# Optimization experiments

Measured on AMD Instinct MI355X. Metric: run time of the kernel, lower is better.

Reference implementation:

```python
import jax, jax.numpy as jnp
import numpy as np
from jax import lax


def _dw_conv(x, w, dilation):
    # depthwise dilated conv along width; x: [B,H,W,C], w: [1,K,1,C] (HWIO, groups=C)
    return lax.conv_general_dilated(
        x, w,
        window_strides=(1, 1),
        padding='SAME',
        rhs_dilation=(1, dilation),
        dimension_numbers=('NHWC', 'HWIO', 'NHWC'),
        feature_group_count=x.shape[-1])


def setup_inputs() -> dict:
    key = jax.random.key(0)
    kx, k1, k2, k3 = jax.random.split(key, 4)
    B, H, W, C = 16, 21, 4096, 64
    K = 8
    scale = 1.0 / np.sqrt(K)  # keep activations O(1) across stages
    x = jax.random.normal(kx, (B, H, W, C), dtype=jnp.float32)
    w1 = jax.random.normal(k1, (1, K, 1, C), dtype=jnp.float32) * scale
    w2 = jax.random.normal(k2, (1, K, 1, C), dtype=jnp.float32) * scale
    w3 = jax.random.normal(k3, (1, K, 1, C), dtype=jnp.float32) * scale
    return {'x': x, 'w1': w1, 'w2': w2, 'w3': w3}


def reference(x, w1, w2, w3):
    # per-channel Conv2D stack == depthwise conv stack; dilations 1, 2, 4; relu after each
    y = jax.nn.relu(_dw_conv(x, w1, 1))
    y = jax.nn.relu(_dw_conv(y, w2, 2))
    y = jax.nn.relu(_dw_conv(y, w3, 4))
    return y
```

## Files before the change

kernel.cpp:

```cpp
#include <hip/hip_runtime.h>


#define W_DIM   4096
#define C_DIM   64
#define L_CHUNK 256
#define NCHUNK  16
#define NROWS   336
#define WAVES_PER_BLOCK 4

#define S1_BODY(j) do {                                                     \
    float a_ = 0.f;                                                         \
    _Pragma("unroll")                                                       \
    for (int k = 0; k < 8; ++k)                                             \
        a_ = fmaf(xf[((j) - 7 + k + 32) & 15], w1r[k], a_);                 \
    s1f[((j) - 4 + 32) & 15] = fmaxf(a_, 0.f);                              \
} while (0)

#define S2_BODY(j) do {                                                     \
    float a_ = 0.f;                                                         \
    _Pragma("unroll")                                                       \
    for (int k = 0; k < 8; ++k)                                             \
        a_ = fmaf(s1f[((j) - 18 + 2 * k + 32) & 15], w2r[k], a_);           \
    s2f[((j) - 11 + 32) & 31] = fmaxf(a_, 0.f);                             \
} while (0)

#define S3_STORE(j, dst) do {                                               \
    float a_ = 0.f;                                                         \
    _Pragma("unroll")                                                       \
    for (int k = 0; k < 8; ++k)                                             \
        a_ = fmaf(s2f[((j) - 39 + 4 * k + 64) & 31], w3r[k], a_);           \
    (dst) = fmaxf(a_, 0.f);                                                 \
} while (0)

__global__ __launch_bounds__(256, 4)
void splitconv_fused_kernel(const float* __restrict__ x,
                            const float* __restrict__ w1,
                            const float* __restrict__ w2,
                            const float* __restrict__ w3,
                            float* __restrict__ out) {
    const int lane  = threadIdx.x & 63;
    const int wid   = threadIdx.x >> 6;
    const int chunk = blockIdx.x & (NCHUNK - 1);
    const int row   = (blockIdx.x >> 4) * WAVES_PER_BLOCK + wid;
    const int w0    = chunk * L_CHUNK;
    const int c     = lane;

    const float* __restrict__ xrow = x   + (size_t)row * (W_DIM * C_DIM) + c;
    float* __restrict__       orow = out + (size_t)row * (W_DIM * C_DIM) + c;

    float w1r[8], w2r[8], w3r[8];
#pragma unroll
    for (int k = 0; k < 8; ++k) {
        w1r[k] = w1[k * C_DIM + c];
        w2r[k] = w2[k * C_DIM + c];
        w3r[k] = w3[k * C_DIM + c];
    }

    float xf[16], s1f[16], s2f[32];
#pragma unroll
    for (int i = 0; i < 16; ++i) { xf[i] = 0.f; s1f[i] = 0.f; }
#pragma unroll
    for (int i = 0; i < 32; ++i) s2f[i] = 0.f;

    if (chunk >= 1 && chunk <= 14) {
        const float* __restrict__ xp = xrow + (size_t)(w0 - 24) * C_DIM;
        float* __restrict__       op = orow + (size_t)w0 * C_DIM;

#pragma unroll
        for (int j = 0; j < 32; ++j) {
            xf[(j + 8) & 15] = xp[j * C_DIM];
            if (j >= 15) S1_BODY(j);
            if (j >= 29) S2_BODY(j);
        }
        xp += 32 * C_DIM;

#pragma unroll
        for (int j = 0; j < 32; ++j) {
            xf[(j + 8) & 15] = xp[j * C_DIM];
            S1_BODY(j);
            S2_BODY(j);
            if (j >= 25) S3_STORE(j, op[(j - 25) * C_DIM]);
        }
        xp += 32 * C_DIM;
        op += 7 * C_DIM;

#pragma unroll 1
        for (int g = 2; g <= 8; ++g) {
#pragma unroll
            for (int j = 0; j < 32; ++j) {
                xf[(j + 8) & 15] = xp[j * C_DIM];
                S1_BODY(j);
                S2_BODY(j);
                S3_STORE(j, op[j * C_DIM]);
            }
            xp += 32 * C_DIM;
            op += 32 * C_DIM;
        }

#pragma unroll
        for (int j = 0; j < 32; ++j) {
            if (j <= 16) xf[(j + 8) & 15] = xp[j * C_DIM];
            if (j <= 24) { S1_BODY(j); S2_BODY(j); }
            if (j <  25) S3_STORE(j, op[j * C_DIM]);
        }
    } else {
        for (int g = 0; g < 10; ++g) {
            const int tbase = w0 - 32 + g * 32;
#pragma unroll
            for (int j = 0; j < 32; ++j) {
                const int t = tbase + j;

                {
                    const int z = t + 8;
                    float xv = 0.f;
                    if (z >= 0 && z < W_DIM && (z - w0) <= L_CHUNK + 24)
                        xv = xrow[(size_t)z * C_DIM];
                    xf[(j + 8) & 15] = xv;
                }

                {
                    const int v = t - 4;
                    float a = 0.f;
#pragma unroll
                    for (int k = 0; k < 8; ++k)
                        a = fmaf(xf[(j - 7 + k + 32) & 15], w1r[k], a);
                    float s = fmaxf(a, 0.f);
                    s1f[(j - 4 + 32) & 15] = (v >= 0 && v < W_DIM) ? s : 0.f;
                }

                {
                    const int u = t - 11;
                    float a = 0.f;
#pragma unroll
                    for (int k = 0; k < 8; ++k)
                        a = fmaf(s1f[(j - 18 + 2 * k + 32) & 15], w2r[k], a);
                    float s = fmaxf(a, 0.f);
                    s2f[(j - 11 + 32) & 31] = (u >= 0 && u < W_DIM) ? s : 0.f;
                }

                {
                    const int wq = t - 25;
                    if (wq >= w0 && wq < w0 + L_CHUNK) {
                        float a = 0.f;
#pragma unroll
                        for (int k = 0; k < 8; ++k)
                            a = fmaf(s2f[(j - 39 + 4 * k + 64) & 31], w3r[k], a);
                        orow[(size_t)wq * C_DIM] = fmaxf(a, 0.f);
                    }
                }
            }
        }
    }
}

extern "C" void kernel_launch(void* const* d_in, const int* in_sizes, int n_in,
                              void* d_out, int out_size, void* d_ws, size_t ws_size,
                              hipStream_t stream) {
    const float* x  = (const float*)d_in[0];
    const float* w1 = (const float*)d_in[1];
    const float* w2 = (const float*)d_in[2];
    const float* w3 = (const float*)d_in[3];
    float* out = (float*)d_out;

    const int totalWaves = NROWS * NCHUNK;
    const int blocks = totalWaves / WAVES_PER_BLOCK;
    splitconv_fused_kernel<<<blocks, 256, 0, stream>>>(x, w1, w2, w3, out);
}
```

Measured before the change: 640.8 us.

## Double-buffer input rows in registers, use nontemporal stores, relax occupancy bound

The interior-chunk path now loads x in full 32-element register tiles (xa/xb ping-pong) one group ahead, replacing the 16-entry ring that fetched each element just before use. This puts more loads in flight to hide global memory latency. Output stores become nontemporal to avoid polluting cache with write-once data. Launch bounds drop from 4 to 3 blocks per CU to give the larger register footprint room, which lowers occupancy.

```diff
diff --git a/kernel.cpp b/kernel.cpp
--- a/kernel.cpp
+++ b/kernel.cpp
@@ -8,11 +8,14 @@
 #define NROWS   336
 #define WAVES_PER_BLOCK 4
 
-#define S1_BODY(j) do {                                                     \
+#define S1X(j, CUR, PRV) do {                                               \
     float a_ = 0.f;                                                         \
     _Pragma("unroll")                                                       \
-    for (int k = 0; k < 8; ++k)                                             \
-        a_ = fmaf(xf[((j) - 7 + k + 32) & 15], w1r[k], a_);                 \
+    for (int k = 0; k < 8; ++k) {                                           \
+        const int i_ = (j) - 7 + k;                                         \
+        const float xv_ = (i_ >= 0) ? CUR[i_ & 31] : PRV[(i_ + 32) & 31];   \
+        a_ = fmaf(xv_, w1r[k], a_);                                         \
+    }                                                                       \
     s1f[((j) - 4 + 32) & 15] = fmaxf(a_, 0.f);                              \
 } while (0)
 
@@ -24,15 +27,15 @@
     s2f[((j) - 11 + 32) & 31] = fmaxf(a_, 0.f);                             \
 } while (0)
 
-#define S3_STORE(j, dst) do {                                               \
+#define S3_NT(j, pdst) do {                                                 \
     float a_ = 0.f;                                                         \
     _Pragma("unroll")                                                       \
     for (int k = 0; k < 8; ++k)                                             \
         a_ = fmaf(s2f[((j) - 39 + 4 * k + 64) & 31], w3r[k], a_);           \
-    (dst) = fmaxf(a_, 0.f);                                                 \
+    __builtin_nontemporal_store(fmaxf(a_, 0.f), (pdst));                    \
 } while (0)
 
-__global__ __launch_bounds__(256, 4)
+__global__ __launch_bounds__(256, 3)
 void splitconv_fused_kernel(const float* __restrict__ x,
                             const float* __restrict__ w1,
                             const float* __restrict__ w2,
@@ -56,54 +59,78 @@
         w3r[k] = w3[k * C_DIM + c];
     }
 
-    float xf[16], s1f[16], s2f[32];
+    float s1f[16], s2f[32];
 #pragma unroll
-    for (int i = 0; i < 16; ++i) { xf[i] = 0.f; s1f[i] = 0.f; }
+    for (int i = 0; i < 16; ++i) s1f[i] = 0.f;
 #pragma unroll
     for (int i = 0; i < 32; ++i) s2f[i] = 0.f;
 
     if (chunk >= 1 && chunk <= 14) {
-        const float* __restrict__ xp = xrow + (size_t)(w0 - 24) * C_DIM;
+        float xa[32], xb[32];
+        const float* __restrict__ xp = xrow + (size_t)(w0 - 32) * C_DIM;
         float* __restrict__       op = orow + (size_t)w0 * C_DIM;
 
 #pragma unroll
+        for (int j = 0; j < 32; ++j) xa[j] = xp[j * C_DIM];
+        xp += 32 * C_DIM;
+
+#pragma unroll
         for (int j = 0; j < 32; ++j) {
-            xf[(j + 8) & 15] = xp[j * C_DIM];
-            if (j >= 15) S1_BODY(j);
+            xb[j] = xp[j * C_DIM];
+            if (j >= 15) S1X(j, xa, xa);
             if (j >= 29) S2_BODY(j);
         }
         xp += 32 * C_DIM;
 
 #pragma unroll
         for (int j = 0; j < 32; ++j) {
-            xf[(j + 8) & 15] = xp[j * C_DIM];
-            S1_BODY(j);
+            xa[j] = xp[j * C_DIM];
+            S1X(j, xb, xa);
             S2_BODY(j);
-            if (j >= 25) S3_STORE(j, op[(j - 25) * C_DIM]);
+            if (j >= 25) S3_NT(j, &op[(j - 25) * C_DIM]);
         }
         xp += 32 * C_DIM;
         op += 7 * C_DIM;
 
 #pragma unroll 1
-        for (int g = 2; g <= 8; ++g) {
+        for (int p = 0; p < 3; ++p) {
 #pragma unroll
             for (int j = 0; j < 32; ++j) {
-                xf[(j + 8) & 15] = xp[j * C_DIM];
-                S1_BODY(j);
+                xb[j] = xp[j * C_DIM];
+                S1X(j, xa, xb);
                 S2_BODY(j);
-                S3_STORE(j, op[j * C_DIM]);
+                S3_NT(j, &op[j * C_DIM]);
             }
-            xp += 32 * C_DIM;
-            op += 32 * C_DIM;
+            xp += 32 * C_DIM; op += 32 * C_DIM;
+#pragma unroll
+            for (int j = 0; j < 32; ++j) {
+                xa[j] = xp[j * C_DIM];
+                S1X(j, xb, xa);
+                S2_BODY(j);
+                S3_NT(j, &op[j * C_DIM]);
+            }
+            xp += 32 * C_DIM; op += 32 * C_DIM;
         }
 
 #pragma unroll
         for (int j = 0; j < 32; ++j) {
-            if (j <= 16) xf[(j + 8) & 15] = xp[j * C_DIM];
-            if (j <= 24) { S1_BODY(j); S2_BODY(j); }
-            if (j <  25) S3_STORE(j, op[j * C_DIM]);
+            if (j <= 24) xb[j] = xp[j * C_DIM];
+            S1X(j, xa, xb);
+            S2_BODY(j);
+            S3_NT(j, &op[j * C_DIM]);
+        }
+        op += 32 * C_DIM;
+
+#pragma unroll
+        for (int j = 0; j < 32; ++j) {
+            if (j <= 24) { S1X(j, xb, xa); S2_BODY(j); }
+            if (j <  25) S3_NT(j, &op[j * C_DIM]);
         }
     } else {
+        float xf[16];
+#pragma unroll
+        for (int i = 0; i < 16; ++i) xf[i] = 0.f;
+
         for (int g = 0; g < 10; ++g) {
             const int tbase = w0 - 32 + g * 32;
 #pragma unroll
@@ -145,7 +172,8 @@
 #pragma unroll
                         for (int k = 0; k < 8; ++k)
                             a = fmaf(s2f[(j - 39 + 4 * k + 64) & 31], w3r[k], a);
-                        orow[(size_t)wq * C_DIM] = fmaxf(a, 0.f);
+                        __builtin_nontemporal_store(fmaxf(a, 0.f),
+                                                    &orow[(size_t)wq * C_DIM]);
                     }
                 }
             }
```

Measured after the change: 635.1 us. Within noise of the previous version (-0.9%).
